# Kernel tuning notes

Hardware: AMD Instinct MI355X
Metric: run time of the kernel (lower is better)

## Reference

```python
import jax, jax.numpy as jnp
import numpy as np

N = 512      # nodes
E = 512      # edges = nb-graph nodes
M = 16384    # nb-graph edges
FIN = 64     # in_node_nf
HID = 128    # hidden_nf
D = 32       # VTV_coord_nf (positional-encoding width)


def _silu(v):
    return v * jax.nn.sigmoid(v)


def _mlp(v, w1, b1, w2, b2):
    # 2-layer MLP with SiLU (matches MLP(in, out, [hidden]))
    return _silu(v @ w1 + b1) @ w2 + b2


def setup_inputs() -> dict:
    key = jax.random.key(0)
    ks = jax.random.split(key, 32)

    def lin(k, i, o, scale=None):
        s = (1.0 / np.sqrt(i)) if scale is None else scale
        return jax.random.normal(k, (i, o), dtype=jnp.float32) * jnp.float32(s)

    inp = {}
    inp['h'] = jax.random.normal(ks[0], (N, FIN), dtype=jnp.float32)
    inp['x'] = jax.random.normal(ks[1], (N, 3), dtype=jnp.float32)
    inp['edges'] = jax.random.randint(ks[2], (2, E), 0, N)
    inp['nb_edge'] = jax.random.randint(ks[3], (2, M), 0, E)
    inp['edge_attr'] = jax.random.normal(ks[4], (E, 4), dtype=jnp.float32)
    inp['nb_num_nodes'] = E  # python int (static)
    # edge_encoder: MLP(2*FIN -> HID -> FIN)
    inp['ew1'] = lin(ks[5], 2 * FIN, HID); inp['eb1'] = jnp.zeros((HID,), jnp.float32)
    inp['ew2'] = lin(ks[6], HID, FIN);     inp['eb2'] = jnp.zeros((FIN,), jnp.float32)
    # PPGN mlp1 / mlp2: MLP(D+FIN -> HID -> FIN)
    inp['p1w1'] = lin(ks[7], D + FIN, HID); inp['p1b1'] = jnp.zeros((HID,), jnp.float32)
    inp['p1w2'] = lin(ks[8], HID, FIN);     inp['p1b2'] = jnp.zeros((FIN,), jnp.float32)
    inp['p2w1'] = lin(ks[9], D + FIN, HID); inp['p2b1'] = jnp.zeros((HID,), jnp.float32)
    inp['p2w2'] = lin(ks[10], HID, FIN);    inp['p2b2'] = jnp.zeros((FIN,), jnp.float32)
    # PPGN output mlp: MLP(D+FIN+FIN -> HID -> FIN) on concat(skip, matmul)
    inp['p3w1'] = lin(ks[11], D + 2 * FIN, HID); inp['p3b1'] = jnp.zeros((HID,), jnp.float32)
    inp['p3w2'] = lin(ks[12], HID, FIN);         inp['p3b2'] = jnp.zeros((FIN,), jnp.float32)
    # IGN 2->1: linear over 5 basis ops
    inp['ign_w'] = lin(ks[13], 5 * FIN, FIN); inp['ign_b'] = jnp.zeros((FIN,), jnp.float32)
    # coord_mlp: Linear(FIN,HID), SiLU, Linear(HID,1,bias=False) with tiny init
    inp['cw1'] = lin(ks[14], FIN, HID); inp['cb1'] = jnp.zeros((HID,), jnp.float32)
    inp['cw2'] = lin(ks[15], HID, 1, scale=0.001)
    # node_dec: MLP(FIN -> HID -> FIN)
    inp['ndw1'] = lin(ks[16], FIN, HID); inp['ndb1'] = jnp.zeros((HID,), jnp.float32)
    inp['ndw2'] = lin(ks[17], HID, FIN); inp['ndb2'] = jnp.zeros((FIN,), jnp.float32)
    return inp


def reference(h, x, edges, nb_edge, edge_attr, nb_num_nodes,
              ew1, eb1, ew2, eb2,
              p1w1, p1b1, p1w2, p1b2,
              p2w1, p2b1, p2w2, p2b2,
              p3w1, p3b1, p3w2, p3b2,
              ign_w, ign_b,
              cw1, cb1, cw2,
              ndw1, ndb1, ndw2, ndb2):
    rows, cols = edges[0], edges[1]
    coord_diff = x[rows] - x[cols]                      # [E,3]
    nbr, nbc = nb_edge[0], nb_edge[1]
    # VTV: inner product of the two relative-position vectors of paired edges
    vtv = jnp.sum(coord_diff[nbr] * coord_diff[nbc], axis=-1)   # [M]
    # sinusoidal positional encoding, a_scale = D/2
    half = D // 2
    div_term = jnp.exp(jnp.log(jnp.float32(10000.0)) * (2.0 * jnp.arange(half, dtype=jnp.float32) / D))
    ang = vtv[:, None] * jnp.float32(D / 2) / div_term          # [M, D/2]
    pe = jnp.stack([jnp.sin(ang), jnp.cos(ang)], axis=-1).reshape(vtv.shape[0], D)
    # node-pair features per original edge
    efn = _mlp(jnp.concatenate([h[rows], h[cols]], axis=1), ew1, eb1, ew2, eb2)  # [E,FIN]
    nb_feat = jnp.concatenate([pe, efn[nbr] * efn[nbc]], axis=1)                 # [M, D+FIN]
    # densify nb-graph 2-tensor and run PPGN block
    En = nb_num_nodes
    T = jnp.zeros((En, En, nb_feat.shape[1]), dtype=nb_feat.dtype).at[nbr, nbc].add(nb_feat)
    m1 = _mlp(T, p1w1, p1b1, p1w2, p1b2)                 # [En,En,FIN]
    m2 = _mlp(T, p2w1, p2b1, p2w2, p2b2)
    mult = jnp.einsum('ikf,kjf->ijf', m1, m2)            # feature-wise matmul
    Tout = _mlp(jnp.concatenate([T, mult], axis=-1), p3w1, p3b1, p3w2, p3b2)
    # IGN 2->1: diag, row-sum, col-sum, total-sum, trace (broadcast)
    idx = jnp.arange(En)
    diag = Tout[idx, idx]                                # [En,FIN]
    rowsum = Tout.sum(axis=1)
    colsum = Tout.sum(axis=0)
    tot = jnp.broadcast_to(Tout.sum(axis=(0, 1)), diag.shape)
    tr = jnp.broadcast_to(diag.sum(axis=0), diag.shape)
    nb_t1 = jnp.concatenate([diag, rowsum, colsum, tot, tr], axis=1) @ ign_w + ign_b  # [En,FIN]
    # coord update: weighted coord_diff, segment-mean over source node
    w = _silu(nb_t1 @ cw1 + cb1) @ cw2                   # [E,1]
    trans = coord_diff * w
    Nn = x.shape[0]
    seg = jax.ops.segment_sum(trans, rows, num_segments=Nn)
    cnt = jax.ops.segment_sum(jnp.ones((rows.shape[0], 1), trans.dtype), rows, num_segments=Nn)
    x_new = x + seg / jnp.clip(cnt, 1.0)
    # node update: scatter_add edge features then residual MLP
    nb_t0 = jax.ops.segment_sum(nb_t1, rows, num_segments=Nn)
    h_new = h + _mlp(nb_t0, ndw1, ndb1, ndw2, ndb2)
    return (h_new, x_new, edge_attr)
```

## Files before the change

### kernel.cpp

```cpp
#include <hip/hip_runtime.h>
#include <hip/hip_bf16.h>

#define NN   512
#define EE   512
#define MM   16384

typedef float v4f __attribute__((ext_vector_type(4)));
typedef short short8v __attribute__((ext_vector_type(8)));

__device__ __forceinline__ float silu_f(float v) { return v / (1.0f + __expf(-v)); }
__device__ __forceinline__ float silu_fast(float v) {
  return v * __builtin_amdgcn_rcpf(1.0f + __expf(-v));
}

__global__ __launch_bounds__(128) void k_front(
    const float* __restrict__ h, const float* __restrict__ x,
    const int* __restrict__ edges, const int* __restrict__ nb_edge,
    const float* __restrict__ ew1, const float* __restrict__ eb1,
    const float* __restrict__ ew2, const float* __restrict__ eb2,
    const float* __restrict__ p1b1, const float* __restrict__ p1w2, const float* __restrict__ p1b2,
    const float* __restrict__ p2b1, const float* __restrict__ p2w2, const float* __restrict__ p2b2,
    const float* __restrict__ p3w1,
    float* __restrict__ coord_diff, float* __restrict__ efn,
    float* __restrict__ c1, float* __restrict__ c2,
    __hip_bfloat16* __restrict__ Wt, int* __restrict__ slotmap) {
  __shared__ float sm[256];
  int b = blockIdx.x, t = threadIdx.x;
  if (b < 512) {
    int r = edges[b], c = edges[EE + b];
    if (t < 3) coord_diff[b * 3 + t] = x[r * 3 + t] - x[c * 3 + t];
    if (t < 64) { sm[t] = h[r * 64 + t]; sm[64 + t] = h[c * 64 + t]; }
    __syncthreads();
    float acc = eb1[t];
    for (int k = 0; k < 128; ++k) acc += sm[k] * ew1[k * 128 + t];
    sm[128 + t] = silu_f(acc);
    __syncthreads();
    if (t < 64) {
      float o = eb2[t];
      for (int k = 0; k < 128; ++k) o += sm[128 + k] * ew2[k * 64 + t];
      efn[b * 64 + t] = o;
    }
  } else if (b == 512) {
    sm[t] = silu_f(p1b1[t]); sm[128 + t] = silu_f(p2b1[t]);
    __syncthreads();
    if (t < 64) {
      float a1 = p1b2[t], a2 = p2b2[t];
      for (int k = 0; k < 128; ++k) { a1 += sm[k] * p1w2[k * 64 + t]; a2 += sm[128 + k] * p2w2[k * 64 + t]; }
      c1[t] = a1; c2[t] = a2;
    }
  } else if (b < 577) {
    int e = (b - 513) * 128 + t;
    int hh = e >> 6, f = e & 63;
    Wt[hh * 64 + f] = __float2bfloat16(p3w1[(96 + f) * 128 + hh]);
  } else {
    int m = (b - 577) * 128 + t;
    int cell = nb_edge[m] * 512 + nb_edge[MM + m];
    atomicCAS(&slotmap[cell], -1, -2);
  }
}

__global__ __launch_bounds__(256) void k_compact(int* __restrict__ slotmap,
                                                 int* __restrict__ slotmapT,
                                                 int* __restrict__ cells,
                                                 int* __restrict__ nC) {
  __shared__ int wbase[4];
  int cell = blockIdx.x * 256 + threadIdx.x;
  int lane = threadIdx.x & 63;
  int wid = threadIdx.x >> 6;
  bool marked = (slotmap[cell] == -2);
  unsigned long long mask = __ballot(marked);
  if (lane == 0) wbase[wid] = __popcll(mask);
  __syncthreads();
  if (threadIdx.x == 0) {
    int tot = wbase[0] + wbase[1] + wbase[2] + wbase[3];
    int base = tot ? atomicAdd(nC, tot) : 0;
    for (int i = 0; i < 4; ++i) { int c = wbase[i]; wbase[i] = base; base += c; }
  }
  __syncthreads();
  if (marked) {
    int rank = __popcll(mask & ((1ull << lane) - 1ull));
    int s = wbase[wid] + rank;
    slotmap[cell] = s;
    slotmapT[(cell & 511) * 512 + (cell >> 9)] = s;
    cells[s] = cell;
  }
}

__global__ __launch_bounds__(192) void k_scatterT(
    const int* __restrict__ nb_edge, const int* __restrict__ slotmap,
    const float* __restrict__ coord_diff, const float* __restrict__ efn,
    float* __restrict__ Tc) {
  int t = threadIdx.x;
  int sub = (t >= 96) ? 1 : 0;
  int c = t - sub * 96;
  int m = blockIdx.x * 2 + sub;
  int a = nb_edge[m], b = nb_edge[MM + m];
  int s = slotmap[a * 512 + b];
  float val;
  if (c < 32) {
    float vtv = coord_diff[a * 3 + 0] * coord_diff[b * 3 + 0]
              + coord_diff[a * 3 + 1] * coord_diff[b * 3 + 1]
              + coord_diff[a * 3 + 2] * coord_diff[b * 3 + 2];
    int i = c >> 1;
    float ang = vtv * 16.0f * __expf(-0.57564627324851143f * (float)i);
    val = (c & 1) ? cosf(ang) : sinf(ang);
  } else {
    int f = c - 32;
    val = efn[a * 64 + f] * efn[b * 64 + f];
  }
  atomicAdd(&Tc[s * 96 + c], val);
}

__global__ __launch_bounds__(256) void k_prep2(
    const float* __restrict__ Tc,
    const float* __restrict__ p3w1, const float* __restrict__ w11,
    const float* __restrict__ w21, const float* __restrict__ w12,
    const float* __restrict__ w22,
    __hip_bfloat16* __restrict__ TcB, __hip_bfloat16* __restrict__ WBT,
    __hip_bfloat16* __restrict__ W2T) {
  int i = blockIdx.x * 256 + threadIdx.x;
  if (i < 16384 * 96) { TcB[i] = __float2bfloat16(Tc[i]); return; }
  i -= 16384 * 96;
  if (i < 384 * 96) {
    int n = i / 96, k = i % 96;
    float v = (n < 128) ? p3w1[k * 128 + n]
            : (n < 256) ? w11[k * 128 + (n - 128)]
                        : w21[k * 128 + (n - 256)];
    WBT[i] = __float2bfloat16(v);
    return;
  }
  i -= 384 * 96;
  {
    int which = i >> 13, rem = i & 8191;
    int n = rem >> 7, k = rem & 127;
    const float* w2 = which ? w22 : w12;
    W2T[i] = __float2bfloat16(w2[k * 64 + n]);
  }
}

__global__ __launch_bounds__(256) void k_gemm1(
    const int* __restrict__ nC, const __hip_bfloat16* __restrict__ TcB,
    const __hip_bfloat16* __restrict__ WBT,
    const float* __restrict__ b11, const float* __restrict__ b21,
    float* __restrict__ TWc, __hip_bfloat16* __restrict__ H1,
    __hip_bfloat16* __restrict__ H2) {
  __shared__ short As[128 * 104];
  __shared__ short Bs[128 * 104];
  int i0 = blockIdx.x * 128;
  int nt = blockIdx.y;
  if (i0 >= *nC) return;
  int t = threadIdx.x;
  int w = t >> 6, lane = t & 63;
  int wy = w >> 1, wx = w & 1;
  int q = lane >> 4, l15 = lane & 15;
  const short* Ap = (const short*)TcB;
  const short* Bp = (const short*)WBT + nt * 128 * 96;
  for (int idx = t; idx < 1536; idx += 256) {
    int row = idx / 12, seg = idx % 12;
    *(short8v*)&As[row * 104 + seg * 8] = *(const short8v*)&Ap[(i0 + row) * 96 + seg * 8];
    *(short8v*)&Bs[row * 104 + seg * 8] = *(const short8v*)&Bp[row * 96 + seg * 8];
  }
  __syncthreads();
  v4f acc[4][4];
#pragma unroll
  for (int yi = 0; yi < 4; ++yi)
#pragma unroll
    for (int xj = 0; xj < 4; ++xj) acc[yi][xj] = (v4f){0.f, 0.f, 0.f, 0.f};
#pragma unroll
  for (int k0 = 0; k0 < 96; k0 += 32) {
    short8v af[4], bf[4];
#pragma unroll
    for (int x = 0; x < 4; ++x) {
      af[x] = *(const short8v*)&As[(wy * 64 + x * 16 + l15) * 104 + k0 + q * 8];
      bf[x] = *(const short8v*)&Bs[(wx * 64 + x * 16 + l15) * 104 + k0 + q * 8];
    }
#pragma unroll
    for (int yi = 0; yi < 4; ++yi)
#pragma unroll
      for (int xj = 0; xj < 4; ++xj)
        acc[yi][xj] = __builtin_amdgcn_mfma_f32_16x16x32_bf16(af[yi], bf[xj], acc[yi][xj], 0, 0, 0);
  }
#pragma unroll
  for (int yi = 0; yi < 4; ++yi)
#pragma unroll
    for (int r = 0; r < 4; ++r) {
      int s = i0 + wy * 64 + yi * 16 + q * 4 + r;
#pragma unroll
      for (int xj = 0; xj < 4; ++xj) {
        int j = wx * 64 + xj * 16 + l15;
        float val = acc[yi][xj][r];
        if (nt == 0) TWc[s * 128 + j] = val;
        else if (nt == 1) H1[s * 128 + j] = __float2bfloat16(silu_f(val + b11[j]));
        else H2[s * 128 + j] = __float2bfloat16(silu_f(val + b21[j]));
      }
    }
}

__global__ __launch_bounds__(256) void k_gemm2(
    const int* __restrict__ nC, const int* __restrict__ cells,
    const __hip_bfloat16* __restrict__ H1, const __hip_bfloat16* __restrict__ H2,
    const __hip_bfloat16* __restrict__ W2T,
    const float* __restrict__ b12, const float* __restrict__ b22,
    const float* __restrict__ c1, const float* __restrict__ c2,
    __hip_bfloat16* __restrict__ Dc1, __hip_bfloat16* __restrict__ Dc2,
    float* __restrict__ A, float* __restrict__ B) {
  __shared__ short Hs[128 * 136];
  __shared__ short Wsh[64 * 136];
  __shared__ int cellL[128];
  int i0 = blockIdx.x * 128;
  int which = blockIdx.y;
  int nc = *nC;
  if (i0 >= nc) return;
  int t = threadIdx.x;
  int w = t >> 6, lane = t & 63;
  int q = lane >> 4, l15 = lane & 15;
  const short* Hp = (const short*)(which ? H2 : H1);
  const short* Wp = (const short*)W2T + which * 64 * 128;
  for (int idx = t; idx < 2048; idx += 256) {
    int row = idx >> 4, seg = idx & 15;
    *(short8v*)&Hs[row * 136 + seg * 8] = *(const short8v*)&Hp[(i0 + row) * 128 + seg * 8];
  }
  for (int idx = t; idx < 1024; idx += 256) {
    int row = idx >> 4, seg = idx & 15;
    *(short8v*)&Wsh[row * 136 + seg * 8] = *(const short8v*)&Wp[row * 128 + seg * 8];
  }
  if (t < 128) cellL[t] = (i0 + t < nc) ? cells[i0 + t] : 0;
  __syncthreads();
  v4f acc[2][4];
#pragma unroll
  for (int y = 0; y < 2; ++y)
#pragma unroll
    for (int xj = 0; xj < 4; ++xj) acc[y][xj] = (v4f){0.f, 0.f, 0.f, 0.f};
#pragma unroll
  for (int k0 = 0; k0 < 128; k0 += 32) {
    short8v af[2], bf[4];
#pragma unroll
    for (int y = 0; y < 2; ++y)
      af[y] = *(const short8v*)&Hs[(w * 32 + y * 16 + l15) * 136 + k0 + q * 8];
#pragma unroll
    for (int xj = 0; xj < 4; ++xj)
      bf[xj] = *(const short8v*)&Wsh[(xj * 16 + l15) * 136 + k0 + q * 8];
#pragma unroll
    for (int y = 0; y < 2; ++y)
#pragma unroll
      for (int xj = 0; xj < 4; ++xj)
        acc[y][xj] = __builtin_amdgcn_mfma_f32_16x16x32_bf16(af[y], bf[xj], acc[y][xj], 0, 0, 0);
  }
  const float* bias = which ? b22 : b12;
  const float* cc = which ? c2 : c1;
#pragma unroll
  for (int y = 0; y < 2; ++y)
#pragma unroll
    for (int r = 0; r < 4; ++r) {
      int lrow = w * 32 + y * 16 + q * 4 + r;
      int s = i0 + lrow;
      if (s >= nc) continue;
      int cell = cellL[lrow];
      int idx = which ? (cell & 511) : (cell >> 9);
#pragma unroll
      for (int xj = 0; xj < 4; ++xj) {
        int hh = xj * 16 + l15;
        float d = acc[y][xj][r] + bias[hh] - cc[hh];
        if (which) { atomicAdd(&B[idx * 64 + hh], d); Dc2[s * 64 + hh] = __float2bfloat16(d); }
        else       { atomicAdd(&A[idx * 64 + hh], d); Dc1[s * 64 + hh] = __float2bfloat16(d); }
      }
    }
}

__global__ __launch_bounds__(128) void k_densify(
    const int* __restrict__ slotmap, const int* __restrict__ slotmapT,
    const __hip_bfloat16* __restrict__ Dc1, const __hip_bfloat16* __restrict__ Dc2,
    __hip_bfloat16* __restrict__ D1d, __hip_bfloat16* __restrict__ D2dT) {
  int b = blockIdx.x;
  int f = b >> 9, row = b & 511;
  int t = threadIdx.x;
  int which = blockIdx.y;
  const int* sm = which ? &slotmapT[row * 512] : &slotmap[row * 512];
  const unsigned short* Dc = (const unsigned short*)(which ? Dc2 : Dc1);
  unsigned short* dst = (unsigned short*)(which ? &D2dT[(f * 512 + row) * 512]
                                                : &D1d[(f * 512 + row) * 512]);
  int4 s4 = *(const int4*)&sm[t * 4];
  ushort4 o;
  o.x = (s4.x >= 0) ? Dc[s4.x * 64 + f] : 0;
  o.y = (s4.y >= 0) ? Dc[s4.y * 64 + f] : 0;
  o.z = (s4.z >= 0) ? Dc[s4.z * 64 + f] : 0;
  o.w = (s4.w >= 0) ? Dc[s4.w * 64 + f] : 0;
  *(ushort4*)&dst[t * 4] = o;
}

__global__ __launch_bounds__(128) void k_uv(
    const float* __restrict__ A, const float* __restrict__ B,
    const float* __restrict__ c1, const float* __restrict__ c2,
    const float* __restrict__ p3w1, const float* __restrict__ p3b1,
    float* __restrict__ u, float* __restrict__ v) {
  __shared__ float vec[64];
  int i = blockIdx.x, y = blockIdx.y, t = threadIdx.x;
  if (t < 64)
    vec[t] = (y == 0) ? (512.0f * c1[t] * c2[t] + c2[t] * A[i * 64 + t])
                      : (c1[t] * B[i * 64 + t]);
  __syncthreads();
  float a = (y == 0) ? p3b1[t] : 0.f;
  for (int f = 0; f < 64; ++f) a += vec[f] * p3w1[(96 + f) * 128 + t];
  (y == 0 ? u : v)[i * 128 + t] = a;
}

__global__ __launch_bounds__(256) void k_einsum_mfma(
    const __hip_bfloat16* __restrict__ D1d,
    const __hip_bfloat16* __restrict__ D2dT,
    __hip_bfloat16* __restrict__ S_fij) {
  __shared__ short As[128 * 40];
  __shared__ short Bs[128 * 40];
  int braw = blockIdx.x;
  int b = (braw & 7) * 128 + (braw >> 3);
  int f = b >> 4;
  int i0 = ((b >> 2) & 3) * 128, j0 = (b & 3) * 128;
  int t = threadIdx.x;
  int w = t >> 6, lane = t & 63;
  int wy = w >> 1, wx = w & 1;
  int q = lane >> 4, l15 = lane & 15;
  const short* Ap = (const short*)D1d + f * 262144;
  const short* Bp = (const short*)D2dT + f * 262144;
  int row = t >> 1, seg = t & 1;
  v4f acc[4][4];
#pragma unroll
  for (int yi = 0; yi < 4; ++yi)
#pragma unroll
    for (int xj = 0; xj < 4; ++xj) acc[yi][xj] = (v4f){0.f, 0.f, 0.f, 0.f};
  for (int k0 = 0; k0 < 512; k0 += 32) {
    __syncthreads();
    const short8v* ga = (const short8v*)&Ap[(i0 + row) * 512 + k0 + seg * 16];
    const short8v* gb = (const short8v*)&Bp[(j0 + row) * 512 + k0 + seg * 16];
    *(short8v*)&As[row * 40 + seg * 16] = ga[0];
    *(short8v*)&As[row * 40 + seg * 16 + 8] = ga[1];
    *(short8v*)&Bs[row * 40 + seg * 16] = gb[0];
    *(short8v*)&Bs[row * 40 + seg * 16 + 8] = gb[1];
    __syncthreads();
    short8v af[4], bf[4];
#pragma unroll
    for (int x = 0; x < 4; ++x) {
      af[x] = *(const short8v*)&As[(wy * 64 + x * 16 + l15) * 40 + q * 8];
      bf[x] = *(const short8v*)&Bs[(wx * 64 + x * 16 + l15) * 40 + q * 8];
    }
#pragma unroll
    for (int yi = 0; yi < 4; ++yi)
#pragma unroll
      for (int xj = 0; xj < 4; ++xj)
        acc[yi][xj] = __builtin_amdgcn_mfma_f32_16x16x32_bf16(af[yi], bf[xj], acc[yi][xj], 0, 0, 0);
  }
#pragma unroll
  for (int yi = 0; yi < 4; ++yi)
#pragma unroll
    for (int r = 0; r < 4; ++r) {
      int irow = i0 + wy * 64 + yi * 16 + q * 4 + r;
#pragma unroll
      for (int xj = 0; xj < 4; ++xj)
        S_fij[(f * 512 + irow) * 512 + j0 + wx * 64 + xj * 16 + l15] =
            __float2bfloat16(acc[yi][xj][r]);
    }
}

__global__ __launch_bounds__(256) void k_transpose(
    const __hip_bfloat16* __restrict__ S_fij, __hip_bfloat16* __restrict__ S) {
  __shared__ short lds[64 * 72];
  int t = threadIdx.x;
  int ij0 = blockIdx.x * 64;
  const short* src = (const short*)S_fij;
#pragma unroll
  for (int p = 0; p < 2; ++p) {
    int f = p * 32 + (t >> 3), seg = t & 7;
    short8v ga = *(const short8v*)&src[f * 262144 + ij0 + seg * 8];
    int fgrp = f >> 3, flo = f & 7;
#pragma unroll
    for (int k = 0; k < 8; ++k) {
      int ij = seg * 8 + k;
      int swz = (fgrp ^ (ij & 7) ^ ((ij >> 3) & 7)) & 7;
      lds[ij * 72 + swz * 8 + flo] = ga[k];
    }
  }
  __syncthreads();
  short* dst = (short*)S;
#pragma unroll
  for (int p = 0; p < 2; ++p) {
    int ij = p * 32 + (t >> 3), fseg = t & 7;
    int swz = (fseg ^ (ij & 7) ^ ((ij >> 3) & 7)) & 7;
    short8v val = *(const short8v*)&lds[ij * 72 + swz * 8];
    *(short8v*)&dst[(ij0 + ij) * 64 + fseg * 8] = val;
  }
}

__global__ __launch_bounds__(256) void k_tout_mfma(
    const __hip_bfloat16* __restrict__ S, const float* __restrict__ u,
    const float* __restrict__ v, const __hip_bfloat16* __restrict__ Wt,
    float* __restrict__ row_part, float* __restrict__ col_part,
    float* __restrict__ diag_silu) {
  __shared__ __hip_bfloat16 WtL[128 * 72];
  __shared__ __hip_bfloat16 uvL[4096];
  __shared__ __hip_bfloat16 colbuf[4][16][140];
  int t = threadIdx.x;
  int w = t >> 6, lane = t & 63;
  int q = lane >> 4, l15 = lane & 15;
  int bi = blockIdx.x >> 5, bj = blockIdx.x & 31;
  int i0 = bi * 16, j0 = bj * 16;
  for (int e = t; e < 4096; e += 256) {
    int row = e >> 5, c2 = e & 31;
    ((unsigned*)WtL)[row * 36 + c2] = ((const unsigned*)Wt)[row * 32 + c2];
  }
  for (int e = t; e < 2048; e += 256)
    uvL[e] = __float2bfloat16(u[(i0 + (e >> 7)) * 128 + (e & 127)]);
  for (int e = t; e < 2048; e += 256)
    uvL[2048 + e] = __float2bfloat16(v[(j0 + (e >> 7)) * 128 + (e & 127)]);
  short8v a[4][2];
#pragma unroll
  for (int mt = 0; mt < 4; ++mt) {
    const short8v* sp =
        (const short8v*)&S[((i0 + w * 4 + mt) * 512 + j0 + l15) * 64];
    a[mt][0] = sp[q];
    a[mt][1] = sp[4 + q];
  }
  __syncthreads();
#pragma unroll
  for (int half = 0; half < 2; ++half) {
    v4f acc[4][4];
#pragma unroll
    for (int mt = 0; mt < 4; ++mt)
#pragma unroll
      for (int n4 = 0; n4 < 4; ++n4) {
        int nt = half * 4 + n4;
        const short8v* b0 = (const short8v*)&WtL[(nt * 16 + l15) * 72 + q * 8];
        const short8v* b1 = (const short8v*)&WtL[(nt * 16 + l15) * 72 + 32 + q * 8];
        v4f c = {0.f, 0.f, 0.f, 0.f};
        c = __builtin_amdgcn_mfma_f32_16x16x32_bf16(a[mt][0], *b0, c, 0, 0, 0);
        c = __builtin_amdgcn_mfma_f32_16x16x32_bf16(a[mt][1], *b1, c, 0, 0, 0);
        acc[mt][n4] = c;
      }
#pragma unroll
    for (int n4 = 0; n4 < 4; ++n4) {
      int nt = half * 4 + n4;
      int hh = nt * 16 + l15;
      float uu[4];
#pragma unroll
      for (int mt = 0; mt < 4; ++mt)
        uu[mt] = __bfloat162float(uvL[(w * 4 + mt) * 128 + hh]);
      float rs[4] = {0.f, 0.f, 0.f, 0.f};
#pragma unroll
      for (int r = 0; r < 4; ++r) {
        int jL = q * 4 + r;
        float cs = 0.f;
        float vv = __bfloat162float(uvL[2048 + jL * 128 + hh]);
#pragma unroll
        for (int mt = 0; mt < 4; ++mt) {
          int iL = w * 4 + mt;
          float sv = silu_fast(acc[mt][n4][r] + uu[mt] + vv);
          rs[mt] += sv;
          cs += sv;
          if (bi == bj && iL == jL) diag_silu[(i0 + iL) * 128 + hh] = sv;
        }
        colbuf[w][jL][hh] = __float2bfloat16(cs);
      }
#pragma unroll
      for (int mt = 0; mt < 4; ++mt) {
        float rsum = rs[mt];
        rsum += __shfl_xor(rsum, 16);
        rsum += __shfl_xor(rsum, 32);
        if (q == 0)
          row_part[(bj * 512 + i0 + w * 4 + mt) * 128 + hh] = rsum;
      }
    }
  }
  __syncthreads();
  for (int e = t; e < 2048; e += 256) {
    int jL = e >> 7, hh = e & 127;
    float acc4 = __bfloat162float(colbuf[0][jL][hh]) + __bfloat162float(colbuf[1][jL][hh]) +
                 __bfloat162float(colbuf[2][jL][hh]) + __bfloat162float(colbuf[3][jL][hh]);
    col_part[(bi * 512 + j0 + jL) * 128 + hh] = acc4;
  }
}

__global__ __launch_bounds__(128) void k_corr(
    const int* __restrict__ cells, const int* __restrict__ nC,
    const __hip_bfloat16* __restrict__ S, const float* __restrict__ u,
    const float* __restrict__ v, const float* __restrict__ TWc,
    const __hip_bfloat16* __restrict__ Wt,
    float* __restrict__ corr_row, float* __restrict__ corr_col,
    float* __restrict__ diag_silu) {
  __shared__ float sf[64];
  int s = blockIdx.x;
  if (s >= *nC) return;
  int t = threadIdx.x;
  int cell = cells[s];
  int ai = cell >> 9, bj = cell & 511;
  if (t < 64) sf[t] = __bfloat162float(S[(ai * 512 + bj) * 64 + t]);
  __syncthreads();
  float acc = 0.f;
  const __hip_bfloat16* wr = &Wt[t * 64];
  for (int f = 0; f < 64; ++f) acc += sf[f] * __bfloat162float(wr[f]);
  float z0 = acc + u[ai * 128 + t] + v[bj * 128 + t];
  float zc = z0 + TWc[s * 128 + t];
  float d = silu_fast(zc) - silu_fast(z0);
  atomicAdd(&corr_row[ai * 128 + t], d);
  atomicAdd(&corr_col[bj * 128 + t], d);
  if (ai == bj) atomicAdd(&diag_silu[ai * 128 + t], d);
}

__global__ __launch_bounds__(128) void k_tout2f(
    const float* __restrict__ diag_silu, const float* __restrict__ row_part,
    const float* __restrict__ col_part,
    const float* __restrict__ corr_row, const float* __restrict__ corr_col,
    const float* __restrict__ w2, const float* __restrict__ b2,
    float* __restrict__ diag_T, float* __restrict__ row_T, float* __restrict__ col_T,
    float* __restrict__ tot, float* __restrict__ tr) {
  __shared__ float in[128];
  int e = blockIdx.x, which = blockIdx.y, t = threadIdx.x;
  float a;
  if (which == 0) {
    a = diag_silu[e * 128 + t];
  } else {
    const float* src = (which == 1) ? row_part : col_part;
    a = (which == 1) ? corr_row[e * 128 + t] : corr_col[e * 128 + t];
    for (int p = 0; p < 32; ++p) a += src[(p * 512 + e) * 128 + t];
  }
  in[t] = a;
  __syncthreads();
  if (t < 64) {
    float o = 0.f;
    for (int k = 0; k < 128; ++k) o += in[k] * w2[k * 64 + t];
    float val = o + b2[t] * ((which == 0) ? 1.0f : 512.0f);
    if (which == 0)      { diag_T[e * 64 + t] = val; atomicAdd(&tr[t], val); }
    else if (which == 1) { row_T[e * 64 + t] = val; atomicAdd(&tot[t], val); }
    else                 { col_T[e * 64 + t] = val; }
  }
}

__global__ __launch_bounds__(128) void k_nbt1_edge(
    const float* __restrict__ diag_T, const float* __restrict__ row_T,
    const float* __restrict__ col_T, const float* __restrict__ tot,
    const float* __restrict__ tr,
    const float* __restrict__ gw, const float* __restrict__ gb,
    const int* __restrict__ edges, const float* __restrict__ coord_diff,
    const float* __restrict__ edge_attr,
    const float* __restrict__ cw1, const float* __restrict__ cb1,
    const float* __restrict__ cw2,
    float* __restrict__ seg, float* __restrict__ cnt, float* __restrict__ nb_t0,
    float* __restrict__ out_ea) {
  __shared__ float in[320];
  __shared__ float nbt[64];
  __shared__ float red[128];
  int e = blockIdx.x, t = threadIdx.x;
  if (t < 64) {
    in[t] = diag_T[e * 64 + t]; in[64 + t] = row_T[e * 64 + t];
    in[128 + t] = col_T[e * 64 + t]; in[192 + t] = tot[t]; in[256 + t] = tr[t];
  }
  __syncthreads();
  if (t < 64) {
    float a = gb[t];
    for (int k = 0; k < 320; ++k) a += in[k] * gw[k * 64 + t];
    nbt[t] = a;
  }
  __syncthreads();
  float a = cb1[t];
  for (int k = 0; k < 64; ++k) a += nbt[k] * cw1[k * 128 + t];
  red[t] = silu_f(a) * cw2[t];
  __syncthreads();
  for (int s2 = 64; s2 > 0; s2 >>= 1) {
    if (t < s2) red[t] += red[t + s2];
    __syncthreads();
  }
  float w = red[0];
  int r = edges[e];
  if (t < 3) atomicAdd(&seg[r * 3 + t], coord_diff[e * 3 + t] * w);
  if (t == 64) atomicAdd(&cnt[r], 1.0f);
  if (t < 64) atomicAdd(&nb_t0[r * 64 + t], nbt[t]);
  if (t < 4) out_ea[e * 4 + t] = edge_attr[e * 4 + t];
}

__global__ __launch_bounds__(128) void k_node_out(
    const float* __restrict__ h, const float* __restrict__ x,
    const float* __restrict__ seg, const float* __restrict__ cnt,
    const float* __restrict__ nb_t0,
    const float* __restrict__ w1, const float* __restrict__ b1,
    const float* __restrict__ w2, const float* __restrict__ b2,
    float* __restrict__ out_h, float* __restrict__ out_x) {
  __shared__ float in[64];
  __shared__ float hs[128];
  int n = blockIdx.x, t = threadIdx.x;
  if (t < 3) {
    float c = cnt[n]; if (c < 1.f) c = 1.f;
    out_x[n * 3 + t] = x[n * 3 + t] + seg[n * 3 + t] / c;
  }
  if (t < 64) in[t] = nb_t0[n * 64 + t];
  __syncthreads();
  float a = b1[t];
  for (int k = 0; k < 64; ++k) a += in[k] * w1[k * 128 + t];
  hs[t] = silu_f(a);
  __syncthreads();
  if (t < 64) {
    float o = b2[t];
    for (int k = 0; k < 128; ++k) o += hs[k] * w2[k * 64 + t];
    out_h[n * 64 + t] = h[n * 64 + t] + o;
  }
}

extern "C" void kernel_launch(void* const* d_in, const int* in_sizes, int n_in,
                              void* d_out, int out_size, void* d_ws, size_t ws_size,
                              hipStream_t stream) {
  (void)in_sizes; (void)n_in; (void)out_size; (void)ws_size;
  const float* h  = (const float*)d_in[0];
  const float* x  = (const float*)d_in[1];
  const int* edges   = (const int*)d_in[2];
  const int* nb_edge = (const int*)d_in[3];
  const float* edge_attr = (const float*)d_in[4];
  const float* ew1 = (const float*)d_in[6],  *eb1 = (const float*)d_in[7];
  const float* ew2 = (const float*)d_in[8],  *eb2 = (const float*)d_in[9];
  const float* p1w1 = (const float*)d_in[10], *p1b1 = (const float*)d_in[11];
  const float* p1w2 = (const float*)d_in[12], *p1b2 = (const float*)d_in[13];
  const float* p2w1 = (const float*)d_in[14], *p2b1 = (const float*)d_in[15];
  const float* p2w2 = (const float*)d_in[16], *p2b2 = (const float*)d_in[17];
  const float* p3w1 = (const float*)d_in[18], *p3b1 = (const float*)d_in[19];
  const float* p3w2 = (const float*)d_in[20], *p3b2 = (const float*)d_in[21];
  const float* ignw = (const float*)d_in[22], *ignb = (const float*)d_in[23];
  const float* cw1 = (const float*)d_in[24], *cb1 = (const float*)d_in[25];
  const float* cw2 = (const float*)d_in[26];
  const float* ndw1 = (const float*)d_in[27], *ndb1 = (const float*)d_in[28];
  const float* ndw2 = (const float*)d_in[29], *ndb2 = (const float*)d_in[30];

  char* ws = (char*)d_ws;
  __hip_bfloat16* D1d  = (__hip_bfloat16*)(ws + 0);
  __hip_bfloat16* S    = (__hip_bfloat16*)(ws + 0);
  __hip_bfloat16* D2dT = (__hip_bfloat16*)(ws + 33554432);
  __hip_bfloat16* S_fij = (__hip_bfloat16*)(ws + 67108864);
  __hip_bfloat16* TcB = (__hip_bfloat16*)(ws + 67108864);
  __hip_bfloat16* H1  = (__hip_bfloat16*)(ws + 70254592);
  __hip_bfloat16* H2  = (__hip_bfloat16*)(ws + 74448896);
  __hip_bfloat16* WBT = (__hip_bfloat16*)(ws + 78643200);
  __hip_bfloat16* W2T = (__hip_bfloat16*)(ws + 78716928);
  float* row_part = (float*)(ws + 100663296);
  float* col_part = (float*)(ws + 117440512);
  float* Tc    = (float*)(ws + 134217728);
  int*   nC    = (int*)(ws + 140509184);
  float* A     = (float*)(ws + 140509200);
  float* B     = (float*)(ws + 140640272);
  float* seg   = (float*)(ws + 140771344);
  float* cnt   = (float*)(ws + 140777488);
  float* nb_t0 = (float*)(ws + 140779536);
  float* tot   = (float*)(ws + 140910608);
  float* tr    = (float*)(ws + 140910864);
  float* corr_row = (float*)(ws + 140911120);
  float* corr_col = (float*)(ws + 141173264);
  int*   slotmap  = (int*)(ws + 141435904);
  int*   slotmapT = (int*)(ws + 142484480);
  int*   cells    = (int*)(ws + 143533056);
  __hip_bfloat16* Dc1 = (__hip_bfloat16*)(ws + 143598592);
  __hip_bfloat16* Dc2 = (__hip_bfloat16*)(ws + 145695744);
  float* TWc      = (float*)(ws + 147792896);
  float* c1       = (float*)(ws + 156181504);
  float* c2       = (float*)(ws + 156181760);
  float* u        = (float*)(ws + 156182016);
  float* v        = (float*)(ws + 156444160);
  float* coord_diff  = (float*)(ws + 156706304);
  float* efn         = (float*)(ws + 156712448);
  float* diag_silu   = (float*)(ws + 156843520);
  float* diag_T      = (float*)(ws + 157105664);
  float* row_T       = (float*)(ws + 157236736);
  float* col_T       = (float*)(ws + 157367808);
  __hip_bfloat16* Wt  = (__hip_bfloat16*)(ws + 157629952);

  float* out_h  = (float*)d_out;
  float* out_x  = out_h + 512 * 64;
  float* out_ea = out_x + 512 * 3;

  hipMemsetAsync(slotmap, 0xFF, 2097152, stream);
  hipMemsetAsync(ws + 134217728, 0, 7217680, stream);

  k_front<<<705, 128, 0, stream>>>(h, x, edges, nb_edge,
                                   ew1, eb1, ew2, eb2,
                                   p1b1, p1w2, p1b2, p2b1, p2w2, p2b2, p3w1,
                                   coord_diff, efn, c1, c2, Wt, slotmap);
  k_compact<<<1024, 256, 0, stream>>>(slotmap, slotmapT, cells, nC);
  k_scatterT<<<8192, 192, 0, stream>>>(nb_edge, slotmap, coord_diff, efn, Tc);
  k_prep2<<<6352, 256, 0, stream>>>(Tc, p3w1, p1w1, p2w1, p1w2, p2w2,
                                    TcB, WBT, W2T);
  k_gemm1<<<dim3(128, 3), 256, 0, stream>>>(nC, TcB, WBT, p1b1, p2b1,
                                            TWc, H1, H2);
  k_gemm2<<<dim3(128, 2), 256, 0, stream>>>(nC, cells, H1, H2, W2T,
                                            p1b2, p2b2, c1, c2,
                                            Dc1, Dc2, A, B);
  k_densify<<<dim3(32768, 2), 128, 0, stream>>>(slotmap, slotmapT, Dc1, Dc2,
                                                D1d, D2dT);
  k_uv<<<dim3(512, 2), 128, 0, stream>>>(A, B, c1, c2, p3w1, p3b1, u, v);
  k_einsum_mfma<<<1024, 256, 0, stream>>>(D1d, D2dT, S_fij);
  k_transpose<<<4096, 256, 0, stream>>>(S_fij, S);
  k_tout_mfma<<<1024, 256, 0, stream>>>(S, u, v, Wt,
                                        row_part, col_part, diag_silu);
  k_corr<<<16384, 128, 0, stream>>>(cells, nC, S, u, v, TWc, Wt,
                                    corr_row, corr_col, diag_silu);
  k_tout2f<<<dim3(512, 3), 128, 0, stream>>>(diag_silu, row_part, col_part,
                                             corr_row, corr_col,
                                             p3w2, p3b2, diag_T, row_T, col_T,
                                             tot, tr);
  k_nbt1_edge<<<512, 128, 0, stream>>>(diag_T, row_T, col_T, tot, tr,
                                       ignw, ignb, edges, coord_diff, edge_attr,
                                       cw1, cb1, cw2, seg, cnt, nb_t0, out_ea);
  k_node_out<<<512, 128, 0, stream>>>(h, x, seg, cnt, nb_t0,
                                      ndw1, ndb1, ndw2, ndb2, out_h, out_x);
}
```

Before: 368.7 us.

## Fuse prep, densify/uv, and correction kernels to cut launches

Weight transposes and bf16 conversion move from k_prep2 into extra blocks of k_front. The Tc fp32-to-bf16 conversion now happens inside k_gemm1's shared-memory load. k_densify and k_uv merge into one launch, and k_corr becomes extra blocks of k_tout, with a separate corr_diag buffer so the diagonal correction no longer races with diag_silu. The aim is fewer kernel launches and one fewer round trip through global memory for Tc, at the cost of mixing heterogeneous blocks in a single grid.

```diff
diff --git a/kernel.cpp b/kernel.cpp
--- a/kernel.cpp
+++ b/kernel.cpp
@@ -11,6 +11,10 @@
 __device__ __forceinline__ float silu_f(float v) { return v / (1.0f + __expf(-v)); }
 __device__ __forceinline__ float silu_fast(float v) {
   return v * __builtin_amdgcn_rcpf(1.0f + __expf(-v));
+}
+__device__ __forceinline__ short bf16bits(float x) {
+  __hip_bfloat16 b = __float2bfloat16(x);
+  return *(short*)&b;
 }
 
 __global__ __launch_bounds__(128) void k_front(
@@ -18,12 +22,16 @@
     const int* __restrict__ edges, const int* __restrict__ nb_edge,
     const float* __restrict__ ew1, const float* __restrict__ eb1,
     const float* __restrict__ ew2, const float* __restrict__ eb2,
-    const float* __restrict__ p1b1, const float* __restrict__ p1w2, const float* __restrict__ p1b2,
-    const float* __restrict__ p2b1, const float* __restrict__ p2w2, const float* __restrict__ p2b2,
+    const float* __restrict__ p1w1, const float* __restrict__ p1b1,
+    const float* __restrict__ p1w2, const float* __restrict__ p1b2,
+    const float* __restrict__ p2w1, const float* __restrict__ p2b1,
+    const float* __restrict__ p2w2, const float* __restrict__ p2b2,
     const float* __restrict__ p3w1,
     float* __restrict__ coord_diff, float* __restrict__ efn,
     float* __restrict__ c1, float* __restrict__ c2,
-    __hip_bfloat16* __restrict__ Wt, int* __restrict__ slotmap) {
+    __hip_bfloat16* __restrict__ Wt, int* __restrict__ slotmap,
+    __hip_bfloat16* __restrict__ WBT, __hip_bfloat16* __restrict__ W2T,
+    float* __restrict__ corr_diag) {
   __shared__ float sm[256];
   int b = blockIdx.x, t = threadIdx.x;
   if (b < 512) {
@@ -52,10 +60,25 @@
     int e = (b - 513) * 128 + t;
     int hh = e >> 6, f = e & 63;
     Wt[hh * 64 + f] = __float2bfloat16(p3w1[(96 + f) * 128 + hh]);
-  } else {
+  } else if (b < 705) {
     int m = (b - 577) * 128 + t;
     int cell = nb_edge[m] * 512 + nb_edge[MM + m];
     atomicCAS(&slotmap[cell], -1, -2);
+  } else if (b < 993) {
+    int i = (b - 705) * 128 + t;
+    int n = i / 96, k = i % 96;
+    float v = (n < 128) ? p3w1[k * 128 + n]
+            : (n < 256) ? p1w1[k * 128 + (n - 128)]
+                        : p2w1[k * 128 + (n - 256)];
+    WBT[i] = __float2bfloat16(v);
+  } else if (b < 1121) {
+    int i = (b - 993) * 128 + t;
+    int which = i >> 13, rem = i & 8191;
+    int n = rem >> 7, k = rem & 127;
+    const float* w2 = which ? p2w2 : p1w2;
+    W2T[i] = __float2bfloat16(w2[k * 64 + n]);
+  } else {
+    ((float4*)corr_diag)[(b - 1121) * 128 + t] = (float4){0.f, 0.f, 0.f, 0.f};
   }
 }
 
@@ -111,35 +134,8 @@
   atomicAdd(&Tc[s * 96 + c], val);
 }
 
-__global__ __launch_bounds__(256) void k_prep2(
-    const float* __restrict__ Tc,
-    const float* __restrict__ p3w1, const float* __restrict__ w11,
-    const float* __restrict__ w21, const float* __restrict__ w12,
-    const float* __restrict__ w22,
-    __hip_bfloat16* __restrict__ TcB, __hip_bfloat16* __restrict__ WBT,
-    __hip_bfloat16* __restrict__ W2T) {
-  int i = blockIdx.x * 256 + threadIdx.x;
-  if (i < 16384 * 96) { TcB[i] = __float2bfloat16(Tc[i]); return; }
-  i -= 16384 * 96;
-  if (i < 384 * 96) {
-    int n = i / 96, k = i % 96;
-    float v = (n < 128) ? p3w1[k * 128 + n]
-            : (n < 256) ? w11[k * 128 + (n - 128)]
-                        : w21[k * 128 + (n - 256)];
-    WBT[i] = __float2bfloat16(v);
-    return;
-  }
-  i -= 384 * 96;
-  {
-    int which = i >> 13, rem = i & 8191;
-    int n = rem >> 7, k = rem & 127;
-    const float* w2 = which ? w22 : w12;
-    W2T[i] = __float2bfloat16(w2[k * 64 + n]);
-  }
-}
-
 __global__ __launch_bounds__(256) void k_gemm1(
-    const int* __restrict__ nC, const __hip_bfloat16* __restrict__ TcB,
+    const int* __restrict__ nC, const float* __restrict__ Tc,
     const __hip_bfloat16* __restrict__ WBT,
     const float* __restrict__ b11, const float* __restrict__ b21,
     float* __restrict__ TWc, __hip_bfloat16* __restrict__ H1,
@@ -153,11 +149,14 @@
   int w = t >> 6, lane = t & 63;
   int wy = w >> 1, wx = w & 1;
   int q = lane >> 4, l15 = lane & 15;
-  const short* Ap = (const short*)TcB;
   const short* Bp = (const short*)WBT + nt * 128 * 96;
   for (int idx = t; idx < 1536; idx += 256) {
     int row = idx / 12, seg = idx % 12;
-    *(short8v*)&As[row * 104 + seg * 8] = *(const short8v*)&Ap[(i0 + row) * 96 + seg * 8];
+    const float4* tp = (const float4*)&Tc[(i0 + row) * 96 + seg * 8];
+    float4 a0 = tp[0], a1 = tp[1];
+    short8v cv = {bf16bits(a0.x), bf16bits(a0.y), bf16bits(a0.z), bf16bits(a0.w),
+                  bf16bits(a1.x), bf16bits(a1.y), bf16bits(a1.z), bf16bits(a1.w)};
+    *(short8v*)&As[row * 104 + seg * 8] = cv;
     *(short8v*)&Bs[row * 104 + seg * 8] = *(const short8v*)&Bp[row * 96 + seg * 8];
   }
   __syncthreads();
@@ -267,41 +266,41 @@
     }
 }
 
-__global__ __launch_bounds__(128) void k_densify(
+__global__ __launch_bounds__(128) void k_dens_uv(
     const int* __restrict__ slotmap, const int* __restrict__ slotmapT,
     const __hip_bfloat16* __restrict__ Dc1, const __hip_bfloat16* __restrict__ Dc2,
-    __hip_bfloat16* __restrict__ D1d, __hip_bfloat16* __restrict__ D2dT) {
-  int b = blockIdx.x;
-  int f = b >> 9, row = b & 511;
-  int t = threadIdx.x;
-  int which = blockIdx.y;
-  const int* sm = which ? &slotmapT[row * 512] : &slotmap[row * 512];
-  const unsigned short* Dc = (const unsigned short*)(which ? Dc2 : Dc1);
-  unsigned short* dst = (unsigned short*)(which ? &D2dT[(f * 512 + row) * 512]
-                                                : &D1d[(f * 512 + row) * 512]);
-  int4 s4 = *(const int4*)&sm[t * 4];
-  ushort4 o;
-  o.x = (s4.x >= 0) ? Dc[s4.x * 64 + f] : 0;
-  o.y = (s4.y >= 0) ? Dc[s4.y * 64 + f] : 0;
-  o.z = (s4.z >= 0) ? Dc[s4.z * 64 + f] : 0;
-  o.w = (s4.w >= 0) ? Dc[s4.w * 64 + f] : 0;
-  *(ushort4*)&dst[t * 4] = o;
-}
-
-__global__ __launch_bounds__(128) void k_uv(
+    __hip_bfloat16* __restrict__ D1d, __hip_bfloat16* __restrict__ D2dT,
     const float* __restrict__ A, const float* __restrict__ B,
     const float* __restrict__ c1, const float* __restrict__ c2,
     const float* __restrict__ p3w1, const float* __restrict__ p3b1,
     float* __restrict__ u, float* __restrict__ v) {
   __shared__ float vec[64];
-  int i = blockIdx.x, y = blockIdx.y, t = threadIdx.x;
-  if (t < 64)
-    vec[t] = (y == 0) ? (512.0f * c1[t] * c2[t] + c2[t] * A[i * 64 + t])
-                      : (c1[t] * B[i * 64 + t]);
-  __syncthreads();
-  float a = (y == 0) ? p3b1[t] : 0.f;
-  for (int f = 0; f < 64; ++f) a += vec[f] * p3w1[(96 + f) * 128 + t];
-  (y == 0 ? u : v)[i * 128 + t] = a;
+  int b = blockIdx.x, t = threadIdx.x;
+  if (b < 65536) {
+    int which = b >> 15, bb = b & 32767;
+    int f = bb >> 9, row = bb & 511;
+    const int* sm = which ? &slotmapT[row * 512] : &slotmap[row * 512];
+    const unsigned short* Dc = (const unsigned short*)(which ? Dc2 : Dc1);
+    unsigned short* dst = (unsigned short*)(which ? &D2dT[(f * 512 + row) * 512]
+                                                  : &D1d[(f * 512 + row) * 512]);
+    int4 s4 = *(const int4*)&sm[t * 4];
+    ushort4 o;
+    o.x = (s4.x >= 0) ? Dc[s4.x * 64 + f] : 0;
+    o.y = (s4.y >= 0) ? Dc[s4.y * 64 + f] : 0;
+    o.z = (s4.z >= 0) ? Dc[s4.z * 64 + f] : 0;
+    o.w = (s4.w >= 0) ? Dc[s4.w * 64 + f] : 0;
+    *(ushort4*)&dst[t * 4] = o;
+  } else {
+    int e = b - 65536;
+    int i = e >> 1, y = e & 1;
+    if (t < 64)
+      vec[t] = (y == 0) ? (512.0f * c1[t] * c2[t] + c2[t] * A[i * 64 + t])
+                        : (c1[t] * B[i * 64 + t]);
+    __syncthreads();
+    float a = (y == 0) ? p3b1[t] : 0.f;
+    for (int f = 0; f < 64; ++f) a += vec[f] * p3w1[(96 + f) * 128 + t];
+    (y == 0 ? u : v)[i * 128 + t] = a;
+  }
 }
 
 __global__ __launch_bounds__(256) void k_einsum_mfma(
@@ -388,18 +387,45 @@
   }
 }
 
-__global__ __launch_bounds__(256) void k_tout_mfma(
+__global__ __launch_bounds__(256) void k_tout(
     const __hip_bfloat16* __restrict__ S, const float* __restrict__ u,
     const float* __restrict__ v, const __hip_bfloat16* __restrict__ Wt,
+    const float* __restrict__ TWc, const int* __restrict__ cells,
+    const int* __restrict__ nC,
     float* __restrict__ row_part, float* __restrict__ col_part,
-    float* __restrict__ diag_silu) {
+    float* __restrict__ diag_silu,
+    float* __restrict__ corr_row, float* __restrict__ corr_col,
+    float* __restrict__ corr_diag) {
   __shared__ __hip_bfloat16 WtL[128 * 72];
   __shared__ __hip_bfloat16 uvL[4096];
   __shared__ __hip_bfloat16 colbuf[4][16][140];
+  __shared__ float sf2[2][64];
+  int blk = blockIdx.x;
   int t = threadIdx.x;
+  if (blk >= 1024) {
+    int sub = t >> 7, tt = t & 127;
+    int s = (blk - 1024) * 2 + sub;
+    bool act = (s < *nC);
+    int cell = act ? cells[s] : 0;
+    int ai = cell >> 9, bj = cell & 511;
+    if (act && tt < 64) sf2[sub][tt] = __bfloat162float(S[(ai * 512 + bj) * 64 + tt]);
+    __syncthreads();
+    if (!act) return;
+    float acc = 0.f;
+    const __hip_bfloat16* wr = &Wt[tt * 64];
+#pragma unroll 8
+    for (int f = 0; f < 64; ++f) acc += sf2[sub][f] * __bfloat162float(wr[f]);
+    float z0 = acc + u[ai * 128 + tt] + v[bj * 128 + tt];
+    float zc = z0 + TWc[s * 128 + tt];
+    float d = silu_fast(zc) - silu_fast(z0);
+    atomicAdd(&corr_row[ai * 128 + tt], d);
+    atomicAdd(&corr_col[bj * 128 + tt], d);
+    if (ai == bj) atomicAdd(&corr_diag[ai * 128 + tt], d);
+    return;
+  }
   int w = t >> 6, lane = t & 63;
   int q = lane >> 4, l15 = lane & 15;
-  int bi = blockIdx.x >> 5, bj = blockIdx.x & 31;
+  int bi = blk >> 5, bj = blk & 31;
   int i0 = bi * 16, j0 = bj * 16;
   for (int e = t; e < 4096; e += 256) {
     int row = e >> 5, c2 = e & 31;
@@ -476,36 +502,11 @@
   }
 }
 
-__global__ __launch_bounds__(128) void k_corr(
-    const int* __restrict__ cells, const int* __restrict__ nC,
-    const __hip_bfloat16* __restrict__ S, const float* __restrict__ u,
-    const float* __restrict__ v, const float* __restrict__ TWc,
-    const __hip_bfloat16* __restrict__ Wt,
-    float* __restrict__ corr_row, float* __restrict__ corr_col,
-    float* __restrict__ diag_silu) {
-  __shared__ float sf[64];
-  int s = blockIdx.x;
-  if (s >= *nC) return;
-  int t = threadIdx.x;
-  int cell = cells[s];
-  int ai = cell >> 9, bj = cell & 511;
-  if (t < 64) sf[t] = __bfloat162float(S[(ai * 512 + bj) * 64 + t]);
-  __syncthreads();
-  float acc = 0.f;
-  const __hip_bfloat16* wr = &Wt[t * 64];
-  for (int f = 0; f < 64; ++f) acc += sf[f] * __bfloat162float(wr[f]);
-  float z0 = acc + u[ai * 128 + t] + v[bj * 128 + t];
-  float zc = z0 + TWc[s * 128 + t];
-  float d = silu_fast(zc) - silu_fast(z0);
-  atomicAdd(&corr_row[ai * 128 + t], d);
-  atomicAdd(&corr_col[bj * 128 + t], d);
-  if (ai == bj) atomicAdd(&diag_silu[ai * 128 + t], d);
-}
-
 __global__ __launch_bounds__(128) void k_tout2f(
     const float* __restrict__ diag_silu, const float* __restrict__ row_part,
     const float* __restrict__ col_part,
     const float* __restrict__ corr_row, const float* __restrict__ corr_col,
+    const float* __restrict__ corr_diag,
     const float* __restrict__ w2, const float* __restrict__ b2,
     float* __restrict__ diag_T, float* __restrict__ row_T, float* __restrict__ col_T,
     float* __restrict__ tot, float* __restrict__ tr) {
@@ -513,7 +514,7 @@
   int e = blockIdx.x, which = blockIdx.y, t = threadIdx.x;
   float a;
   if (which == 0) {
-    a = diag_silu[e * 128 + t];
+    a = diag_silu[e * 128 + t] + corr_diag[e * 128 + t];
   } else {
     const float* src = (which == 1) ? row_part : col_part;
     a = (which == 1) ? corr_row[e * 128 + t] : corr_col[e * 128 + t];
@@ -628,7 +629,6 @@
   __hip_bfloat16* S    = (__hip_bfloat16*)(ws + 0);
   __hip_bfloat16* D2dT = (__hip_bfloat16*)(ws + 33554432);
   __hip_bfloat16* S_fij = (__hip_bfloat16*)(ws + 67108864);
-  __hip_bfloat16* TcB = (__hip_bfloat16*)(ws + 67108864);
   __hip_bfloat16* H1  = (__hip_bfloat16*)(ws + 70254592);
   __hip_bfloat16* H2  = (__hip_bfloat16*)(ws + 74448896);
   __hip_bfloat16* WBT = (__hip_bfloat16*)(ws + 78643200);
@@ -663,6 +663,7 @@
   float* row_T       = (float*)(ws + 157236736);
   float* col_T       = (float*)(ws + 157367808);
   __hip_bfloat16* Wt  = (__hip_bfloat16*)(ws + 157629952);
+  float* corr_diag   = (float*)(ws + 157646336);
 
   float* out_h  = (float*)d_out;
   float* out_x  = out_h + 512 * 64;
@@ -671,30 +672,28 @@
   hipMemsetAsync(slotmap, 0xFF, 2097152, stream);
   hipMemsetAsync(ws + 134217728, 0, 7217680, stream);
 
-  k_front<<<705, 128, 0, stream>>>(h, x, edges, nb_edge,
-                                   ew1, eb1, ew2, eb2,
-                                   p1b1, p1w2, p1b2, p2b1, p2w2, p2b2, p3w1,
-                                   coord_diff, efn, c1, c2, Wt, slotmap);
+  k_front<<<1633, 128, 0, stream>>>(h, x, edges, nb_edge,
+                                    ew1, eb1, ew2, eb2,
+                                    p1w1, p1b1, p1w2, p1b2,
+                                    p2w1, p2b1, p2w2, p2b2, p3w1,
+                                    coord_diff, efn, c1, c2, Wt, slotmap,
+                                    WBT, W2T, corr_diag);
   k_compact<<<1024, 256, 0, stream>>>(slotmap, slotmapT, cells, nC);
   k_scatterT<<<8192, 192, 0, stream>>>(nb_edge, slotmap, coord_diff, efn, Tc);
-  k_prep2<<<6352, 256, 0, stream>>>(Tc, p3w1, p1w1, p2w1, p1w2, p2w2,
-                                    TcB, WBT, W2T);
-  k_gemm1<<<dim3(128, 3), 256, 0, stream>>>(nC, TcB, WBT, p1b1, p2b1,
+  k_gemm1<<<dim3(128, 3), 256, 0, stream>>>(nC, Tc, WBT, p1b1, p2b1,
                                             TWc, H1, H2);
   k_gemm2<<<dim3(128, 2), 256, 0, stream>>>(nC, cells, H1, H2, W2T,
                                             p1b2, p2b2, c1, c2,
                                             Dc1, Dc2, A, B);
-  k_densify<<<dim3(32768, 2), 128, 0, stream>>>(slotmap, slotmapT, Dc1, Dc2,
-                                                D1d, D2dT);
-  k_uv<<<dim3(512, 2), 128, 0, stream>>>(A, B, c1, c2, p3w1, p3b1, u, v);
+  k_dens_uv<<<66560, 128, 0, stream>>>(slotmap, slotmapT, Dc1, Dc2, D1d, D2dT,
+                                       A, B, c1, c2, p3w1, p3b1, u, v);
   k_einsum_mfma<<<1024, 256, 0, stream>>>(D1d, D2dT, S_fij);
   k_transpose<<<4096, 256, 0, stream>>>(S_fij, S);
-  k_tout_mfma<<<1024, 256, 0, stream>>>(S, u, v, Wt,
-                                        row_part, col_part, diag_silu);
-  k_corr<<<16384, 128, 0, stream>>>(cells, nC, S, u, v, TWc, Wt,
-                                    corr_row, corr_col, diag_silu);
+  k_tout<<<9216, 256, 0, stream>>>(S, u, v, Wt, TWc, cells, nC,
+                                   row_part, col_part, diag_silu,
+                                   corr_row, corr_col, corr_diag);
   k_tout2f<<<dim3(512, 3), 128, 0, stream>>>(diag_silu, row_part, col_part,
-                                             corr_row, corr_col,
+                                             corr_row, corr_col, corr_diag,
                                              p3w2, p3b2, diag_T, row_T, col_T,
                                              tot, tr);
   k_nbt1_edge<<<512, 128, 0, stream>>>(diag_T, row_T, col_T, tot, tr,
```

Result: faster. 361.1 us (-2.0%).
